# Optimization experiments

Hardware: AMD Instinct MI355X
Metric: run time of the kernel (lower is better)

The kernel has to match this reference:

```python
import jax, jax.numpy as jnp
import numpy as np

N_NODES = 100000
F_DIM = 128      # graph.num_node_features
TE_DIM = 32      # te_emb_dim
D = F_DIM + TE_DIM  # attention embed_dim = 160
B = 4096         # number of target nodes (batched python loop)
K = 64           # candidates per target
TAU = 1.0
THRESHOLD = 0.2
EPS = 1e-10


def setup_inputs() -> dict:
    key = jax.random.key(0)
    ks = jax.random.split(key, 16)
    inp = {
        "x": jax.random.normal(ks[0], (N_NODES, F_DIM), dtype=jnp.float32),
        "target_node_ids": jax.random.randint(ks[1], (B,), 0, N_NODES),
        "target_node_times": jax.random.randint(ks[2], (B,), 1, 10000),
        "neighbor_ids": jax.random.randint(ks[3], (B, K), 0, N_NODES),
        "edge_time": jax.random.randint(ks[4], (B, K), 0, 10000),
        "edge_weight": jax.random.uniform(ks[5], (B, K), dtype=jnp.float32),
        "gumbel_u": jax.random.uniform(ks[6], (B, K), dtype=jnp.float32),
        # TemporalEncoding params: te(t) = cos(t * w + b)
        "te_w": jax.random.normal(ks[7], (TE_DIM,), dtype=jnp.float32),
        "te_b": jax.random.normal(ks[8], (TE_DIM,), dtype=jnp.float32),
        # MultiheadAttention params (packed qkv like torch)
        "in_proj_w": jax.random.normal(ks[9], (3 * D, D), dtype=jnp.float32) / np.sqrt(D),
        "in_proj_b": jnp.zeros((3 * D,), dtype=jnp.float32),
        "out_w": jax.random.normal(ks[10], (D, D), dtype=jnp.float32) / np.sqrt(D),
        "out_b": jnp.zeros((D,), dtype=jnp.float32),
        # MLP: Linear(D+1 -> 1) + LeakyReLU
        "mlp_w": jax.random.normal(ks[11], (D + 1,), dtype=jnp.float32) / np.sqrt(D + 1),
        "mlp_b": jnp.zeros((1,), dtype=jnp.float32),
    }
    return inp


def reference(x, target_node_ids, target_node_times, neighbor_ids, edge_time,
              edge_weight, gumbel_u, te_w, te_b, in_proj_w, in_proj_b,
              out_w, out_b, mlp_w, mlp_b):
    # --- build target embedding: [B, D]
    t_x = x[target_node_ids]                                          # [B, F]
    t_te = jnp.cos(target_node_times[:, None].astype(jnp.float32) * te_w + te_b)  # [B, TE]
    q_in = jnp.concatenate([t_x, t_te], axis=-1)                      # [B, D]

    # --- candidate embeddings: [B, K, D]
    c_x = x[neighbor_ids]                                             # [B, K, F]
    c_te = jnp.cos(edge_time[..., None].astype(jnp.float32) * te_w + te_b)        # [B, K, TE]
    kv_in = jnp.concatenate([c_x, c_te], axis=-1)                     # [B, K, D]

    # --- single-head MultiheadAttention (eval mode, 1 query per target)
    Wq, Wk, Wv = in_proj_w[:D], in_proj_w[D:2 * D], in_proj_w[2 * D:]
    bq, bk, bv = in_proj_b[:D], in_proj_b[D:2 * D], in_proj_b[2 * D:]
    q = q_in @ Wq.T + bq                                              # [B, D]
    k = jnp.einsum('bkf,df->bkd', kv_in, Wk) + bk                     # [B, K, D]
    v = jnp.einsum('bkf,df->bkd', kv_in, Wv) + bv                     # [B, K, D]
    scores = jnp.einsum('bd,bkd->bk', q, k) / jnp.sqrt(jnp.float32(D))
    attn_w = jax.nn.softmax(scores, axis=-1)                          # [B, K]
    ctx = jnp.einsum('bk,bkd->bd', attn_w, v)                         # [B, D]
    attn_output = ctx @ out_w.T + out_b                               # [B, D]

    # --- gumbel-softmax mask over attention weights (soft, then threshold)
    g = -jnp.log(-jnp.log(gumbel_u + EPS) + EPS)                      # gumbel(0,1)
    y_soft = jax.nn.softmax((attn_w + g) / TAU, axis=-1)
    candidate_mask = y_soft > THRESHOLD                               # [B, K] bool

    # --- MLP edge-weight update: Linear(D+1 -> 1) + LeakyReLU
    mlp_in = jnp.concatenate(
        [jnp.broadcast_to(attn_output[:, None, :], (attn_output.shape[0], edge_weight.shape[1], attn_output.shape[1])),
         edge_weight[..., None]], axis=-1)                            # [B, K, D+1]
    new_edge_weight = jax.nn.leaky_relu(jnp.einsum('bkf,f->bk', mlp_in, mlp_w) + mlp_b[0])  # [B, K]

    return attn_output, new_edge_weight, candidate_mask
```

## Files before the change

kernel.cpp:

```cpp
#include <hip/hip_runtime.h>

#define F_DIM 128
#define TE_DIM 32
#define DD 160
#define NB 4096
#define KK 64
#define ROWS 4
#define LD 164
#define TE_STRIDE 36

#define WS_M   0
#define WS_V2  25600
#define WS_C   51200
#define WS_U   51360
#define WS_B2  51520
#define WS_S0  51680
#define WS_TE  51684
#define TAB_T  10000
#define TAB_N  (TAB_T * TE_DIM)
#define TAB_BLOCKS 250
#define SETUP_BASE (2 * DD + 3)

__device__ __forceinline__ float dot4acc(const float4 w, const float4 v, float a) {
    a = fmaf(w.x, v.x, a);
    a = fmaf(w.y, v.y, a);
    a = fmaf(w.z, v.z, a);
    a = fmaf(w.w, v.w, a);
    return a;
}

__device__ __forceinline__ float wave_max(float v) {
    #pragma unroll
    for (int off = 32; off > 0; off >>= 1) v = fmaxf(v, __shfl_xor(v, off, 64));
    return v;
}
__device__ __forceinline__ float wave_sum(float v) {
    #pragma unroll
    for (int off = 32; off > 0; off >>= 1) v += __shfl_xor(v, off, 64);
    return v;
}

__device__ __forceinline__ void gemv_rows(
    const float* __restrict__ W, const float* __restrict__ bias,
    const float (*vin)[LD], float (*vout)[LD], int tid)
{
    const int r  = tid & 3;
    const int dl = tid >> 2;
    const float4* v4 = (const float4*)vin[r];
    const float4* w0 = (const float4*)(W + (long)dl * DD);
    const float4* w1 = (const float4*)(W + (long)(dl + 64) * DD);
    float a0 = bias[dl];
    float a1 = bias[dl + 64];
    if (dl < 32) {
        const float4* w2 = (const float4*)(W + (long)(dl + 128) * DD);
        float a2 = bias[dl + 128];
        #pragma unroll 8
        for (int f = 0; f < 40; ++f) {
            const float4 v = v4[f];
            a0 = dot4acc(w0[f], v, a0);
            a1 = dot4acc(w1[f], v, a1);
            a2 = dot4acc(w2[f], v, a2);
        }
        vout[r][dl]       = a0;
        vout[r][dl + 64]  = a1;
        vout[r][dl + 128] = a2;
    } else {
        #pragma unroll 8
        for (int f = 0; f < 40; ++f) {
            const float4 v = v4[f];
            a0 = dot4acc(w0[f], v, a0);
            a1 = dot4acc(w1[f], v, a1);
        }
        vout[r][dl]      = a0;
        vout[r][dl + 64] = a1;
    }
}

__global__ __launch_bounds__(256)
void setup_kernel(const float* __restrict__ ipw, const float* __restrict__ ipb,
                  const float* __restrict__ ow,  const float* __restrict__ ob,
                  const float* __restrict__ te_w, const float* __restrict__ te_b,
                  float* __restrict__ ws)
{
    const int blk = blockIdx.x;
    const int t   = threadIdx.x;
    const float inv = 0.07905694150420949f;

    __shared__ float s_vec[DD];

    if (blk >= SETUP_BASE) {
        const int g0 = (blk - SETUP_BASE) * 256 + t;
        #pragma unroll
        for (int it = 0; it < 5; ++it) {
            const int g = g0 + it * (TAB_BLOCKS * 256);
            const int tt = g >> 5, d = g & 31;
            ws[WS_TE + g] = cosf(fmaf((float)tt, te_w[d], te_b[d]));
        }
        return;
    }

    if (blk < DD) {
        const float* wk = ipw + DD * DD;
        if (t < DD) s_vec[t] = wk[(long)t * DD + blk];
        __syncthreads();
        if (t < DD) {
            float a0 = 0.f, a1 = 0.f, a2 = 0.f, a3 = 0.f;
            #pragma unroll 4
            for (int d = 0; d < DD; d += 4) {
                a0 = fmaf(s_vec[d],     ipw[(long)d * DD + t],       a0);
                a1 = fmaf(s_vec[d + 1], ipw[(long)(d + 1) * DD + t], a1);
                a2 = fmaf(s_vec[d + 2], ipw[(long)(d + 2) * DD + t], a2);
                a3 = fmaf(s_vec[d + 3], ipw[(long)(d + 3) * DD + t], a3);
            }
            ws[WS_M + blk * DD + t] = (a0 + a1 + a2 + a3) * inv;
        }
    } else if (blk < 2 * DD) {
        const int i = blk - DD;
        const float* wv = ipw + 2 * DD * DD;
        if (t < DD) s_vec[t] = ow[(long)i * DD + t];
        __syncthreads();
        if (t < DD) {
            float a0 = 0.f, a1 = 0.f, a2 = 0.f, a3 = 0.f;
            #pragma unroll 4
            for (int d = 0; d < DD; d += 4) {
                a0 = fmaf(s_vec[d],     wv[(long)d * DD + t],       a0);
                a1 = fmaf(s_vec[d + 1], wv[(long)(d + 1) * DD + t], a1);
                a2 = fmaf(s_vec[d + 2], wv[(long)(d + 2) * DD + t], a2);
                a3 = fmaf(s_vec[d + 3], wv[(long)(d + 3) * DD + t], a3);
            }
            ws[WS_V2 + i * DD + t] = a0 + a1 + a2 + a3;
        }
    } else if (blk == 2 * DD) {
        const float* wk = ipw + DD * DD;
        if (t < DD) s_vec[t] = ipb[t];
        __syncthreads();
        if (t < DD) {
            float a0 = 0.f, a1 = 0.f, a2 = 0.f, a3 = 0.f;
            #pragma unroll 4
            for (int d = 0; d < DD; d += 4) {
                a0 = fmaf(s_vec[d],     wk[(long)d * DD + t],       a0);
                a1 = fmaf(s_vec[d + 1], wk[(long)(d + 1) * DD + t], a1);
                a2 = fmaf(s_vec[d + 2], wk[(long)(d + 2) * DD + t], a2);
                a3 = fmaf(s_vec[d + 3], wk[(long)(d + 3) * DD + t], a3);
            }
            ws[WS_C + t] = (a0 + a1 + a2 + a3) * inv;
        }
    } else if (blk == 2 * DD + 1) {
        if (t < DD) s_vec[t] = ipb[DD + t];
        __syncthreads();
        if (t < DD) {
            float a0 = 0.f, a1 = 0.f, a2 = 0.f, a3 = 0.f;
            #pragma unroll 4
            for (int d = 0; d < DD; d += 4) {
                a0 = fmaf(s_vec[d],     ipw[(long)d * DD + t],       a0);
                a1 = fmaf(s_vec[d + 1], ipw[(long)(d + 1) * DD + t], a1);
                a2 = fmaf(s_vec[d + 2], ipw[(long)(d + 2) * DD + t], a2);
                a3 = fmaf(s_vec[d + 3], ipw[(long)(d + 3) * DD + t], a3);
            }
            ws[WS_U + t] = (a0 + a1 + a2 + a3) * inv;
        }
    } else {
        if (t < DD) s_vec[t] = ipb[2 * DD + t];
        __syncthreads();
        if (t < DD) {
            const float* owr = ow + (long)t * DD;
            float a0 = 0.f, a1 = 0.f, a2 = 0.f, a3 = 0.f;
            #pragma unroll 4
            for (int d = 0; d < DD; d += 4) {
                a0 = fmaf(s_vec[d],     owr[d],     a0);
                a1 = fmaf(s_vec[d + 1], owr[d + 1], a1);
                a2 = fmaf(s_vec[d + 2], owr[d + 2], a2);
                a3 = fmaf(s_vec[d + 3], owr[d + 3], a3);
            }
            ws[WS_B2 + t] = ob[t] + (a0 + a1 + a2 + a3);
        }
        if (t >= 192) {
            const int lane = t - 192;
            float p = ipb[lane] * ipb[DD + lane];
            p = fmaf(ipb[lane + 64], ipb[DD + lane + 64], p);
            if (lane < 32) p = fmaf(ipb[lane + 128], ipb[DD + lane + 128], p);
            const float s = wave_sum(p);
            if (lane == 0) ws[WS_S0] = s * inv;
        }
    }
}

__global__ __launch_bounds__(256, 4)
void structure_learner_kernel(
    const float* __restrict__ x,
    const int*   __restrict__ target_node_ids,
    const int*   __restrict__ target_node_times,
    const int*   __restrict__ neighbor_ids,
    const int*   __restrict__ edge_time,
    const float* __restrict__ edge_weight,
    const float* __restrict__ gumbel_u,
    const float* __restrict__ te_w,
    const float* __restrict__ te_b,
    const float* __restrict__ mlp_w,
    const float* __restrict__ mlp_b,
    const float* __restrict__ ws,
    const float* __restrict__ tetab,
    float* __restrict__ out_ao,
    float* __restrict__ out_new,
    float* __restrict__ out_mask)
{
    __shared__ __attribute__((aligned(16))) float s_qin[ROWS][LD];
    __shared__ __attribute__((aligned(16))) float s_qt[ROWS][LD];
    __shared__ __attribute__((aligned(16))) float s_wkv[ROWS][LD];
    __shared__ __attribute__((aligned(16))) float s_ao[ROWS][LD];
    __shared__ float s_attnw[ROWS][KK];
    __shared__ int   s_nid[ROWS][KK];
    __shared__ __attribute__((aligned(4))) _Float16 s_te[ROWS][KK][TE_STRIDE];

    const int tid  = threadIdx.x;
    const int wr   = tid >> 6;
    const int lane = tid & 63;
    const int b    = blockIdx.x * ROWS + wr;

    const float* Mw = ws + WS_M;
    const float* V2 = ws + WS_V2;
    const float* Cv = ws + WS_C;
    const float* Uv = ws + WS_U;
    const float* B2 = ws + WS_B2;
    const float  s0 = ws[WS_S0];

    {
        s_nid[wr][lane] = neighbor_ids[(long)b * KK + lane];
        const int etv_i = edge_time[(long)b * KK + lane];
        const int tn = target_node_ids[b];
        const float2 tx = *(const float2*)(x + (long)tn * F_DIM + lane * 2);
        s_qin[wr][lane * 2]     = tx.x;
        s_qin[wr][lane * 2 + 1] = tx.y;
        if (lane < TE_DIM) {
            const int tt = target_node_times[b];
            s_qin[wr][F_DIM + lane] =
                (tetab && (unsigned)tt < (unsigned)TAB_T)
                    ? tetab[(long)tt * TE_DIM + lane]
                    : cosf(fmaf((float)tt, te_w[lane], te_b[lane]));
        }
        if (tetab && (unsigned)etv_i < (unsigned)TAB_T) {
            const float4* trow = (const float4*)(tetab + (long)etv_i * TE_DIM);
            #pragma unroll
            for (int jj = 0; jj < 8; ++jj) {
                const float4 tv = trow[jj];
                union { _Float16 h[2]; unsigned u; } p0, p1;
                p0.h[0] = (_Float16)tv.x; p0.h[1] = (_Float16)tv.y;
                p1.h[0] = (_Float16)tv.z; p1.h[1] = (_Float16)tv.w;
                *(unsigned*)&s_te[wr][lane][4 * jj]     = p0.u;
                *(unsigned*)&s_te[wr][lane][4 * jj + 2] = p1.u;
            }
        } else {
            const float etv = (float)etv_i;
            #pragma unroll
            for (int jj = 0; jj < 16; ++jj) {
                union { _Float16 h[2]; unsigned u; } pk;
                pk.h[0] = (_Float16)cosf(fmaf(etv, te_w[2 * jj],     te_b[2 * jj]));
                pk.h[1] = (_Float16)cosf(fmaf(etv, te_w[2 * jj + 1], te_b[2 * jj + 1]));
                *(unsigned*)&s_te[wr][lane][2 * jj] = pk.u;
            }
        }
    }
    __syncthreads();

    gemv_rows(Mw, Cv, s_qin, s_qt, tid);
    __syncthreads();

    float aw;
    {
        float p = s_qin[wr][lane] * Uv[lane];
        p = fmaf(s_qin[wr][lane + 64], Uv[lane + 64], p);
        if (lane < 32) p = fmaf(s_qin[wr][128 + lane], Uv[128 + lane], p);
        const float sbk = wave_sum(p) + s0;

        const int nidk = s_nid[wr][lane];
        const float4* xr  = (const float4*)(x + (long)nidk * F_DIM);
        const float4* qt4 = (const float4*)s_qt[wr];
        float acc0 = 0.f, acc1 = 0.f;
        #pragma unroll 16
        for (int f = 0; f < F_DIM / 8; ++f) {
            acc0 = dot4acc(xr[2 * f],     qt4[2 * f],     acc0);
            acc1 = dot4acc(xr[2 * f + 1], qt4[2 * f + 1], acc1);
        }
        float acc = acc0 + acc1;
        const float* qte = s_qt[wr] + F_DIM;
        #pragma unroll
        for (int jj = 0; jj < 16; ++jj) {
            union { _Float16 h[2]; unsigned u; } pk;
            pk.u = *(const unsigned*)&s_te[wr][lane][2 * jj];
            acc = fmaf(qte[2 * jj],     (float)pk.h[0], acc);
            acc = fmaf(qte[2 * jj + 1], (float)pk.h[1], acc);
        }
        const float sc = acc + sbk;
        const float m = wave_max(sc);
        const float e = expf(sc - m);
        const float l = wave_sum(e);
        aw = e / l;
        s_attnw[wr][lane] = aw;
    }

    {
        float ax = 0.f, ay = 0.f, at = 0.f;
        const float* xb = x + lane * 2;
        const int lte = lane & 31;
        #pragma unroll 16
        for (int k = 0; k < KK; ++k) {
            const float wgt = s_attnw[wr][k];
            const int   nid = s_nid[wr][k];
            const float2 xv = *(const float2*)(xb + (long)nid * F_DIM);
            ax = fmaf(wgt, xv.x, ax);
            ay = fmaf(wgt, xv.y, ay);
            at = fmaf(wgt, (float)s_te[wr][k][lte], at);
        }
        s_wkv[wr][lane * 2]     = ax;
        s_wkv[wr][lane * 2 + 1] = ay;
        if (lane < TE_DIM) s_wkv[wr][F_DIM + lane] = at;
    }
    __syncthreads();

    gemv_rows(V2, B2, s_wkv, s_ao, tid);
    __syncthreads();

    {
        float p = s_ao[wr][lane] * mlp_w[lane];
        p = fmaf(s_ao[wr][lane + 64], mlp_w[lane + 64], p);
        if (lane < 32) p = fmaf(s_ao[wr][lane + 128], mlp_w[lane + 128], p);
        const float base = wave_sum(p) + mlp_b[0];

        float* ao = out_ao + (long)b * DD;
        ao[lane]      = s_ao[wr][lane];
        ao[lane + 64] = s_ao[wr][lane + 64];
        if (lane < 32) ao[lane + 128] = s_ao[wr][lane + 128];

        const float u = gumbel_u[(long)b * KK + lane];
        const float g = -logf(-logf(u + 1e-10f) + 1e-10f);
        const float z = aw + g;
        const float m = wave_max(z);
        const float e = expf(z - m);
        const float l = wave_sum(e);
        out_mask[(long)b * KK + lane] = (e / l > 0.2f) ? 1.0f : 0.0f;

        const float ew  = edge_weight[(long)b * KK + lane];
        const float val = fmaf(ew, mlp_w[DD], base);
        out_new[(long)b * KK + lane] = (val >= 0.f) ? val : 0.01f * val;
    }
}

extern "C" void kernel_launch(void* const* d_in, const int* in_sizes, int n_in,
                              void* d_out, int out_size, void* d_ws, size_t ws_size,
                              hipStream_t stream) {
    const float* x   = (const float*)d_in[0];
    const int*   tni = (const int*)d_in[1];
    const int*   tnt = (const int*)d_in[2];
    const int*   nid = (const int*)d_in[3];
    const int*   et  = (const int*)d_in[4];
    const float* ew  = (const float*)d_in[5];
    const float* gu  = (const float*)d_in[6];
    const float* tew = (const float*)d_in[7];
    const float* teb = (const float*)d_in[8];
    const float* ipw = (const float*)d_in[9];
    const float* ipb = (const float*)d_in[10];
    const float* ow  = (const float*)d_in[11];
    const float* ob  = (const float*)d_in[12];
    const float* mw  = (const float*)d_in[13];
    const float* mb  = (const float*)d_in[14];

    float* wsf = (float*)d_ws;

    float* out      = (float*)d_out;
    float* out_ao   = out;
    float* out_new  = out + (long)NB * DD;
    float* out_mask = out + (long)NB * DD + (long)NB * KK;

    const bool use_tab = ws_size >= (size_t)(WS_TE + TAB_N) * sizeof(float);
    const int  setup_grid = SETUP_BASE + (use_tab ? TAB_BLOCKS : 0);

    setup_kernel<<<setup_grid, 256, 0, stream>>>(ipw, ipb, ow, ob, tew, teb, wsf);

    structure_learner_kernel<<<NB / ROWS, 256, 0, stream>>>(
        x, tni, tnt, nid, et, ew, gu, tew, teb, mw, mb, wsf,
        use_tab ? (wsf + WS_TE) : nullptr,
        out_ao, out_new, out_mask);
}
```

Before: 175.4 us.

## Software-pipeline neighbor row gathers across barriers and GEMV phases

The first chunk of each candidate's feature row is prefetched into registers before the barrier and first GEMV, and the rest is loaded in double-buffered chunks. The weighted-sum gather over neighbors is issued in batches of eight, with the first batch launched before the softmax reductions. The gumbel and edge-weight loads are hoisted ahead of the second GEMV. The aim is to hide global-memory gather latency behind compute and synchronisation, at the cost of higher register pressure that may reduce occupancy.

After: 175.8 us. No clear change (+0.2%).

```diff
diff --git a/kernel.cpp b/kernel.cpp
--- a/kernel.cpp
+++ b/kernel.cpp
@@ -224,8 +224,9 @@
     const float* B2 = ws + WS_B2;
     const float  s0 = ws[WS_S0];
 
+    const int nidk = neighbor_ids[(long)b * KK + lane];
     {
-        s_nid[wr][lane] = neighbor_ids[(long)b * KK + lane];
+        s_nid[wr][lane] = nidk;
         const int etv_i = edge_time[(long)b * KK + lane];
         const int tn = target_node_ids[b];
         const float2 tx = *(const float2*)(x + (long)tn * F_DIM + lane * 2);
@@ -260,6 +261,12 @@
             }
         }
     }
+
+    const float4* xr = (const float4*)(x + (long)nidk * F_DIM);
+    float4 cA[8];
+    #pragma unroll
+    for (int j = 0; j < 8; ++j) cA[j] = xr[j];
+
     __syncthreads();
 
     gemv_rows(Mw, Cv, s_qin, s_qt, tid);
@@ -267,21 +274,44 @@
 
     float aw;
     {
+        float4 cB[8];
+        #pragma unroll
+        for (int j = 0; j < 8; ++j) cB[j] = xr[8 + j];
+
         float p = s_qin[wr][lane] * Uv[lane];
         p = fmaf(s_qin[wr][lane + 64], Uv[lane + 64], p);
         if (lane < 32) p = fmaf(s_qin[wr][128 + lane], Uv[128 + lane], p);
         const float sbk = wave_sum(p) + s0;
 
-        const int nidk = s_nid[wr][lane];
-        const float4* xr  = (const float4*)(x + (long)nidk * F_DIM);
         const float4* qt4 = (const float4*)s_qt[wr];
         float acc0 = 0.f, acc1 = 0.f;
-        #pragma unroll 16
-        for (int f = 0; f < F_DIM / 8; ++f) {
-            acc0 = dot4acc(xr[2 * f],     qt4[2 * f],     acc0);
-            acc1 = dot4acc(xr[2 * f + 1], qt4[2 * f + 1], acc1);
+
+        #pragma unroll
+        for (int j = 0; j < 8; j += 2) {
+            acc0 = dot4acc(cA[j],     qt4[j],     acc0);
+            acc1 = dot4acc(cA[j + 1], qt4[j + 1], acc1);
+        }
+        #pragma unroll
+        for (int j = 0; j < 8; ++j) cA[j] = xr[16 + j];
+        #pragma unroll
+        for (int j = 0; j < 8; j += 2) {
+            acc0 = dot4acc(cB[j],     qt4[8 + j], acc0);
+            acc1 = dot4acc(cB[j + 1], qt4[9 + j], acc1);
+        }
+        #pragma unroll
+        for (int j = 0; j < 8; ++j) cB[j] = xr[24 + j];
+        #pragma unroll
+        for (int j = 0; j < 8; j += 2) {
+            acc0 = dot4acc(cA[j],     qt4[16 + j], acc0);
+            acc1 = dot4acc(cA[j + 1], qt4[17 + j], acc1);
+        }
+        #pragma unroll
+        for (int j = 0; j < 8; j += 2) {
+            acc0 = dot4acc(cB[j],     qt4[24 + j], acc0);
+            acc1 = dot4acc(cB[j + 1], qt4[25 + j], acc1);
         }
         float acc = acc0 + acc1;
+
         const float* qte = s_qt[wr] + F_DIM;
         #pragma unroll
         for (int jj = 0; jj < 16; ++jj) {
@@ -291,31 +321,47 @@
             acc = fmaf(qte[2 * jj + 1], (float)pk.h[1], acc);
         }
         const float sc = acc + sbk;
+
+        const float* xb = x + lane * 2;
+        float2 vc[8];
+        #pragma unroll
+        for (int j = 0; j < 8; ++j)
+            vc[j] = *(const float2*)(xb + (long)s_nid[wr][j] * F_DIM);
+
         const float m = wave_max(sc);
         const float e = expf(sc - m);
         const float l = wave_sum(e);
         aw = e / l;
         s_attnw[wr][lane] = aw;
-    }
-
-    {
+
         float ax = 0.f, ay = 0.f, at = 0.f;
-        const float* xb = x + lane * 2;
         const int lte = lane & 31;
-        #pragma unroll 16
-        for (int k = 0; k < KK; ++k) {
-            const float wgt = s_attnw[wr][k];
-            const int   nid = s_nid[wr][k];
-            const float2 xv = *(const float2*)(xb + (long)nid * F_DIM);
-            ax = fmaf(wgt, xv.x, ax);
-            ay = fmaf(wgt, xv.y, ay);
-            at = fmaf(wgt, (float)s_te[wr][k][lte], at);
+        #pragma unroll
+        for (int c = 0; c < 8; ++c) {
+            float2 vn[8];
+            if (c < 7) {
+                #pragma unroll
+                for (int j = 0; j < 8; ++j)
+                    vn[j] = *(const float2*)(xb + (long)s_nid[wr][(c + 1) * 8 + j] * F_DIM);
+            }
+            #pragma unroll
+            for (int j = 0; j < 8; ++j) {
+                const int k = c * 8 + j;
+                const float wgt = s_attnw[wr][k];
+                ax = fmaf(wgt, vc[j].x, ax);
+                ay = fmaf(wgt, vc[j].y, ay);
+                at = fmaf(wgt, (float)s_te[wr][k][lte], at);
+                if (c < 7) vc[j] = vn[j];
+            }
         }
         s_wkv[wr][lane * 2]     = ax;
         s_wkv[wr][lane * 2 + 1] = ay;
         if (lane < TE_DIM) s_wkv[wr][F_DIM + lane] = at;
     }
     __syncthreads();
+
+    const float u  = gumbel_u[(long)b * KK + lane];
+    const float ew = edge_weight[(long)b * KK + lane];
 
     gemv_rows(V2, B2, s_wkv, s_ao, tid);
     __syncthreads();
@@ -331,7 +377,6 @@
         ao[lane + 64] = s_ao[wr][lane + 64];
         if (lane < 32) ao[lane + 128] = s_ao[wr][lane + 128];
 
-        const float u = gumbel_u[(long)b * KK + lane];
         const float g = -logf(-logf(u + 1e-10f) + 1e-10f);
         const float z = aw + g;
         const float m = wave_max(z);
@@ -339,7 +384,6 @@
         const float l = wave_sum(e);
         out_mask[(long)b * KK + lane] = (e / l > 0.2f) ? 1.0f : 0.0f;
 
-        const float ew  = edge_weight[(long)b * KK + lane];
         const float val = fmaf(ew, mlp_w[DD], base);
         out_new[(long)b * KK + lane] = (val >= 0.f) ? val : 0.01f * val;
     }
```

## Split each target row across two waves with cross-wave softmax merge

Applied to the files above, without the earlier changes.

Each block now handles 2 target rows instead of 4, and each row is split across two waves. Each wave covers 32 candidates, with lane pairs splitting the feature dot products, and the two halves' softmax max and sum are merged through shared memory. The weighted-value sums are kept as two partial vectors that are added inside the output GEMV. This doubles the block count and raises the occupancy hint to 8, aiming to improve latency hiding for the gathered neighbor loads. The cost is extra __syncthreads and shared-memory reductions, plus each block re-reading the GEMV weights for fewer rows.

Result: slower. 234.5 us (+33.7%).

```diff
diff --git a/kernel.cpp b/kernel.cpp
--- a/kernel.cpp
+++ b/kernel.cpp
@@ -5,7 +5,7 @@
 #define DD 160
 #define NB 4096
 #define KK 64
-#define ROWS 4
+#define ROWS 2
 #define LD 164
 #define TE_STRIDE 36
 
@@ -44,35 +44,62 @@
     const float* __restrict__ W, const float* __restrict__ bias,
     const float (*vin)[LD], float (*vout)[LD], int tid)
 {
-    const int r  = tid & 3;
-    const int dl = tid >> 2;
+    const int r  = tid & 1;
+    const int dl = tid >> 1;
     const float4* v4 = (const float4*)vin[r];
     const float4* w0 = (const float4*)(W + (long)dl * DD);
-    const float4* w1 = (const float4*)(W + (long)(dl + 64) * DD);
     float a0 = bias[dl];
-    float a1 = bias[dl + 64];
     if (dl < 32) {
-        const float4* w2 = (const float4*)(W + (long)(dl + 128) * DD);
-        float a2 = bias[dl + 128];
+        const float4* w1 = (const float4*)(W + (long)(dl + 128) * DD);
+        float a1 = bias[dl + 128];
         #pragma unroll 8
         for (int f = 0; f < 40; ++f) {
             const float4 v = v4[f];
             a0 = dot4acc(w0[f], v, a0);
             a1 = dot4acc(w1[f], v, a1);
-            a2 = dot4acc(w2[f], v, a2);
         }
         vout[r][dl]       = a0;
-        vout[r][dl + 64]  = a1;
-        vout[r][dl + 128] = a2;
+        vout[r][dl + 128] = a1;
     } else {
         #pragma unroll 8
         for (int f = 0; f < 40; ++f) {
             const float4 v = v4[f];
             a0 = dot4acc(w0[f], v, a0);
+        }
+        vout[r][dl] = a0;
+    }
+}
+
+__device__ __forceinline__ void gemv_rows2(
+    const float* __restrict__ W, const float* __restrict__ bias,
+    const float (*vin)[2][LD], float (*vout)[LD], int tid)
+{
+    const int r  = tid & 1;
+    const int dl = tid >> 1;
+    const float4* va = (const float4*)vin[r][0];
+    const float4* vb = (const float4*)vin[r][1];
+    const float4* w0 = (const float4*)(W + (long)dl * DD);
+    float a0 = bias[dl];
+    if (dl < 32) {
+        const float4* w1 = (const float4*)(W + (long)(dl + 128) * DD);
+        float a1 = bias[dl + 128];
+        #pragma unroll 8
+        for (int f = 0; f < 40; ++f) {
+            const float4 A = va[f], B = vb[f];
+            float4 v; v.x = A.x + B.x; v.y = A.y + B.y; v.z = A.z + B.z; v.w = A.w + B.w;
+            a0 = dot4acc(w0[f], v, a0);
             a1 = dot4acc(w1[f], v, a1);
         }
-        vout[r][dl]      = a0;
-        vout[r][dl + 64] = a1;
+        vout[r][dl]       = a0;
+        vout[r][dl + 128] = a1;
+    } else {
+        #pragma unroll 8
+        for (int f = 0; f < 40; ++f) {
+            const float4 A = va[f], B = vb[f];
+            float4 v; v.x = A.x + B.x; v.y = A.y + B.y; v.z = A.z + B.z; v.w = A.w + B.w;
+            a0 = dot4acc(w0[f], v, a0);
+        }
+        vout[r][dl] = a0;
     }
 }
 
@@ -185,7 +212,7 @@
     }
 }
 
-__global__ __launch_bounds__(256, 4)
+__global__ __launch_bounds__(256, 8)
 void structure_learner_kernel(
     const float* __restrict__ x,
     const int*   __restrict__ target_node_ids,
@@ -206,15 +233,22 @@
 {
     __shared__ __attribute__((aligned(16))) float s_qin[ROWS][LD];
     __shared__ __attribute__((aligned(16))) float s_qt[ROWS][LD];
-    __shared__ __attribute__((aligned(16))) float s_wkv[ROWS][LD];
+    __shared__ __attribute__((aligned(16))) float s_wkvh[ROWS][2][LD];
     __shared__ __attribute__((aligned(16))) float s_ao[ROWS][LD];
     __shared__ float s_attnw[ROWS][KK];
     __shared__ int   s_nid[ROWS][KK];
     __shared__ __attribute__((aligned(4))) _Float16 s_te[ROWS][KK][TE_STRIDE];
+    __shared__ float2 s_red[ROWS][2];
+    __shared__ float2 s_red2[ROWS][2];
 
     const int tid  = threadIdx.x;
-    const int wr   = tid >> 6;
+    const int w    = tid >> 6;
     const int lane = tid & 63;
+    const int wr   = w >> 1;
+    const int h    = w & 1;
+    const int kk   = lane >> 1;
+    const int j    = lane & 1;
+    const int k    = h * 32 + kk;
     const int b    = blockIdx.x * ROWS + wr;
 
     const float* Mw = ws + WS_M;
@@ -225,38 +259,44 @@
     const float  s0 = ws[WS_S0];
 
     {
-        s_nid[wr][lane] = neighbor_ids[(long)b * KK + lane];
-        const int etv_i = edge_time[(long)b * KK + lane];
-        const int tn = target_node_ids[b];
-        const float2 tx = *(const float2*)(x + (long)tn * F_DIM + lane * 2);
-        s_qin[wr][lane * 2]     = tx.x;
-        s_qin[wr][lane * 2 + 1] = tx.y;
-        if (lane < TE_DIM) {
+        if (lane < 32) {
+            const int km = h * 32 + lane;
+            s_nid[wr][km] = neighbor_ids[(long)b * KK + km];
+        }
+        if (h == 0) {
+            const int tn = target_node_ids[b];
+            const float2 tx = *(const float2*)(x + (long)tn * F_DIM + lane * 2);
+            s_qin[wr][lane * 2]     = tx.x;
+            s_qin[wr][lane * 2 + 1] = tx.y;
+        } else if (lane < TE_DIM) {
             const int tt = target_node_times[b];
             s_qin[wr][F_DIM + lane] =
                 (tetab && (unsigned)tt < (unsigned)TAB_T)
                     ? tetab[(long)tt * TE_DIM + lane]
                     : cosf(fmaf((float)tt, te_w[lane], te_b[lane]));
         }
+        const int etv_i = edge_time[(long)b * KK + k];
         if (tetab && (unsigned)etv_i < (unsigned)TAB_T) {
-            const float4* trow = (const float4*)(tetab + (long)etv_i * TE_DIM);
+            const float4* trow = (const float4*)(tetab + (long)etv_i * TE_DIM) + 4 * j;
             #pragma unroll
-            for (int jj = 0; jj < 8; ++jj) {
-                const float4 tv = trow[jj];
-                union { _Float16 h[2]; unsigned u; } p0, p1;
-                p0.h[0] = (_Float16)tv.x; p0.h[1] = (_Float16)tv.y;
-                p1.h[0] = (_Float16)tv.z; p1.h[1] = (_Float16)tv.w;
-                *(unsigned*)&s_te[wr][lane][4 * jj]     = p0.u;
-                *(unsigned*)&s_te[wr][lane][4 * jj + 2] = p1.u;
+            for (int q = 0; q < 4; ++q) {
+                const float4 tv = trow[q];
+                const int jj = 4 * j + q;
+                union { _Float16 h2[2]; unsigned u; } p0, p1;
+                p0.h2[0] = (_Float16)tv.x; p0.h2[1] = (_Float16)tv.y;
+                p1.h2[0] = (_Float16)tv.z; p1.h2[1] = (_Float16)tv.w;
+                *(unsigned*)&s_te[wr][k][4 * jj]     = p0.u;
+                *(unsigned*)&s_te[wr][k][4 * jj + 2] = p1.u;
             }
         } else {
             const float etv = (float)etv_i;
             #pragma unroll
-            for (int jj = 0; jj < 16; ++jj) {
-                union { _Float16 h[2]; unsigned u; } pk;
-                pk.h[0] = (_Float16)cosf(fmaf(etv, te_w[2 * jj],     te_b[2 * jj]));
-                pk.h[1] = (_Float16)cosf(fmaf(etv, te_w[2 * jj + 1], te_b[2 * jj + 1]));
-                *(unsigned*)&s_te[wr][lane][2 * jj] = pk.u;
+            for (int q = 0; q < 8; ++q) {
+                const int d0 = 16 * j + 2 * q;
+                union { _Float16 h2[2]; unsigned u; } pk;
+                pk.h2[0] = (_Float16)cosf(fmaf(etv, te_w[d0],     te_b[d0]));
+                pk.h2[1] = (_Float16)cosf(fmaf(etv, te_w[d0 + 1], te_b[d0 + 1]));
+                *(unsigned*)&s_te[wr][k][d0] = pk.u;
             }
         }
     }
@@ -265,83 +305,107 @@
     gemv_rows(Mw, Cv, s_qin, s_qt, tid);
     __syncthreads();
 
-    float aw;
+    float e_loc, m_h;
     {
         float p = s_qin[wr][lane] * Uv[lane];
         p = fmaf(s_qin[wr][lane + 64], Uv[lane + 64], p);
         if (lane < 32) p = fmaf(s_qin[wr][128 + lane], Uv[128 + lane], p);
         const float sbk = wave_sum(p) + s0;
 
-        const int nidk = s_nid[wr][lane];
-        const float4* xr  = (const float4*)(x + (long)nidk * F_DIM);
-        const float4* qt4 = (const float4*)s_qt[wr];
+        const int nidk = s_nid[wr][k];
+        const float4* xr  = (const float4*)(x + (long)nidk * F_DIM) + 16 * j;
+        const float4* qt4 = (const float4*)s_qt[wr] + 16 * j;
         float acc0 = 0.f, acc1 = 0.f;
-        #pragma unroll 16
-        for (int f = 0; f < F_DIM / 8; ++f) {
-            acc0 = dot4acc(xr[2 * f],     qt4[2 * f],     acc0);
-            acc1 = dot4acc(xr[2 * f + 1], qt4[2 * f + 1], acc1);
+        #pragma unroll 8
+        for (int f = 0; f < 16; f += 2) {
+            acc0 = dot4acc(xr[f],     qt4[f],     acc0);
+            acc1 = dot4acc(xr[f + 1], qt4[f + 1], acc1);
         }
         float acc = acc0 + acc1;
-        const float* qte = s_qt[wr] + F_DIM;
+        const float* qte = s_qt[wr] + F_DIM + 16 * j;
         #pragma unroll
-        for (int jj = 0; jj < 16; ++jj) {
-            union { _Float16 h[2]; unsigned u; } pk;
-            pk.u = *(const unsigned*)&s_te[wr][lane][2 * jj];
-            acc = fmaf(qte[2 * jj],     (float)pk.h[0], acc);
-            acc = fmaf(qte[2 * jj + 1], (float)pk.h[1], acc);
-        }
+        for (int ii = 0; ii < 8; ++ii) {
+            union { _Float16 h2[2]; unsigned u; } pk;
+            pk.u = *(const unsigned*)&s_te[wr][k][16 * j + 2 * ii];
+            acc = fmaf(qte[2 * ii],     (float)pk.h2[0], acc);
+            acc = fmaf(qte[2 * ii + 1], (float)pk.h2[1], acc);
+        }
+        acc += __shfl_xor(acc, 1, 64);
         const float sc = acc + sbk;
-        const float m = wave_max(sc);
-        const float e = expf(sc - m);
-        const float l = wave_sum(e);
-        aw = e / l;
-        s_attnw[wr][lane] = aw;
-    }
-
+        m_h = wave_max(sc);
+        e_loc = expf(sc - m_h);
+        const float l_h = wave_sum(e_loc) * 0.5f;
+        if (lane == 0) s_red[wr][h] = make_float2(m_h, l_h);
+    }
+    __syncthreads();
+
+    float aw;
     {
+        const float2 R0 = s_red[wr][0], R1 = s_red[wr][1];
+        const float m = fmaxf(R0.x, R1.x);
+        const float l = R0.y * expf(R0.x - m) + R1.y * expf(R1.x - m);
+        aw = e_loc * expf(m_h - m) / l;
+        if (j == 0) s_attnw[wr][k] = aw;
+
         float ax = 0.f, ay = 0.f, at = 0.f;
         const float* xb = x + lane * 2;
         const int lte = lane & 31;
-        #pragma unroll 16
-        for (int k = 0; k < KK; ++k) {
-            const float wgt = s_attnw[wr][k];
-            const int   nid = s_nid[wr][k];
+        #pragma unroll 8
+        for (int q = 0; q < 32; ++q) {
+            const int kq = 32 * h + q;
+            const float wgt = s_attnw[wr][kq];
+            const int   nid = s_nid[wr][kq];
             const float2 xv = *(const float2*)(xb + (long)nid * F_DIM);
             ax = fmaf(wgt, xv.x, ax);
             ay = fmaf(wgt, xv.y, ay);
-            at = fmaf(wgt, (float)s_te[wr][k][lte], at);
-        }
-        s_wkv[wr][lane * 2]     = ax;
-        s_wkv[wr][lane * 2 + 1] = ay;
-        if (lane < TE_DIM) s_wkv[wr][F_DIM + lane] = at;
-    }
-    __syncthreads();
-
-    gemv_rows(V2, B2, s_wkv, s_ao, tid);
-    __syncthreads();
-
+            at = fmaf(wgt, (float)s_te[wr][kq][lte], at);
+        }
+        s_wkvh[wr][h][lane * 2]     = ax;
+        s_wkvh[wr][h][lane * 2 + 1] = ay;
+        if (lane < TE_DIM) s_wkvh[wr][h][F_DIM + lane] = at;
+    }
+    __syncthreads();
+
+    const float u  = gumbel_u[(long)b * KK + k];
+    const float ew = edge_weight[(long)b * KK + k];
+
+    gemv_rows2(V2, B2, s_wkvh, s_ao, tid);
+    __syncthreads();
+
+    float base, y_e, y_mh;
     {
         float p = s_ao[wr][lane] * mlp_w[lane];
         p = fmaf(s_ao[wr][lane + 64], mlp_w[lane + 64], p);
         if (lane < 32) p = fmaf(s_ao[wr][lane + 128], mlp_w[lane + 128], p);
-        const float base = wave_sum(p) + mlp_b[0];
+        base = wave_sum(p) + mlp_b[0];
 
         float* ao = out_ao + (long)b * DD;
-        ao[lane]      = s_ao[wr][lane];
-        ao[lane + 64] = s_ao[wr][lane + 64];
-        if (lane < 32) ao[lane + 128] = s_ao[wr][lane + 128];
-
-        const float u = gumbel_u[(long)b * KK + lane];
+        if (h == 0) {
+            ao[lane] = s_ao[wr][lane];
+            if (lane < 32) ao[128 + lane] = s_ao[wr][128 + lane];
+        } else {
+            ao[64 + lane] = s_ao[wr][64 + lane];
+        }
+
         const float g = -logf(-logf(u + 1e-10f) + 1e-10f);
         const float z = aw + g;
-        const float m = wave_max(z);
-        const float e = expf(z - m);
-        const float l = wave_sum(e);
-        out_mask[(long)b * KK + lane] = (e / l > 0.2f) ? 1.0f : 0.0f;
-
-        const float ew  = edge_weight[(long)b * KK + lane];
-        const float val = fmaf(ew, mlp_w[DD], base);
-        out_new[(long)b * KK + lane] = (val >= 0.f) ? val : 0.01f * val;
+        y_mh = wave_max(z);
+        y_e  = expf(z - y_mh);
+        const float l_h = wave_sum(y_e) * 0.5f;
+        if (lane == 0) s_red2[wr][h] = make_float2(y_mh, l_h);
+    }
+    __syncthreads();
+
+    {
+        const float2 R0 = s_red2[wr][0], R1 = s_red2[wr][1];
+        const float m = fmaxf(R0.x, R1.x);
+        const float l = R0.y * expf(R0.x - m) + R1.y * expf(R1.x - m);
+        const float y = y_e * expf(y_mh - m) / l;
+        if (j == 0) {
+            out_mask[(long)b * KK + k] = (y > 0.2f) ? 1.0f : 0.0f;
+            const float val = fmaf(ew, mlp_w[DD], base);
+            out_new[(long)b * KK + k] = (val >= 0.f) ? val : 0.01f * val;
+        }
     }
 }
 
```

## Fuse score and weighted-sum passes with online softmax over fp16 staged neighbor tiles

Applied to the files above, without the earlier changes.

The kernel now processes candidates in tiles of 16, with 4 lanes per candidate. Each neighbor's x row and temporal encoding is loaded from global memory once, used for the score dot product, and staged as fp16 in shared memory for the attention-weighted accumulation. An online-softmax rescale replaces the separate full softmax, and the second global gather of x rows is gone. In exchange it adds block-wide syncs per tile, rounds x to fp16 in the context sum, and reconstructs the attention weights afterwards for the gumbel mask.

After: 162.4 us, median of 2. 7.4% less time.

```diff
diff --git a/kernel.cpp b/kernel.cpp
--- a/kernel.cpp
+++ b/kernel.cpp
@@ -7,7 +7,8 @@
 #define KK 64
 #define ROWS 4
 #define LD 164
-#define TE_STRIDE 36
+#define XH_STRIDE 168
+#define KT 16
 
 #define WS_M   0
 #define WS_V2  25600
@@ -204,13 +205,15 @@
     float* __restrict__ out_new,
     float* __restrict__ out_mask)
 {
+    __shared__ __attribute__((aligned(16))) _Float16 s_xh[ROWS][KT][XH_STRIDE];
     __shared__ __attribute__((aligned(16))) float s_qin[ROWS][LD];
     __shared__ __attribute__((aligned(16))) float s_qt[ROWS][LD];
     __shared__ __attribute__((aligned(16))) float s_wkv[ROWS][LD];
     __shared__ __attribute__((aligned(16))) float s_ao[ROWS][LD];
-    __shared__ float s_attnw[ROWS][KK];
+    __shared__ float s_aw[ROWS][KK];
+    __shared__ float s_mt[ROWS][4];
     __shared__ int   s_nid[ROWS][KK];
-    __shared__ __attribute__((aligned(4))) _Float16 s_te[ROWS][KK][TE_STRIDE];
+    __shared__ int   s_et[ROWS][KK];
 
     const int tid  = threadIdx.x;
     const int wr   = tid >> 6;
@@ -225,8 +228,9 @@
     const float  s0 = ws[WS_S0];
 
     {
-        s_nid[wr][lane] = neighbor_ids[(long)b * KK + lane];
-        const int etv_i = edge_time[(long)b * KK + lane];
+        const long eb = (long)b * KK + lane;
+        s_nid[wr][lane] = neighbor_ids[eb];
+        s_et[wr][lane]  = edge_time[eb];
         const int tn = target_node_ids[b];
         const float2 tx = *(const float2*)(x + (long)tn * F_DIM + lane * 2);
         s_qin[wr][lane * 2]     = tx.x;
@@ -238,108 +242,137 @@
                     ? tetab[(long)tt * TE_DIM + lane]
                     : cosf(fmaf((float)tt, te_w[lane], te_b[lane]));
         }
-        if (tetab && (unsigned)etv_i < (unsigned)TAB_T) {
-            const float4* trow = (const float4*)(tetab + (long)etv_i * TE_DIM);
-            #pragma unroll
-            for (int jj = 0; jj < 8; ++jj) {
-                const float4 tv = trow[jj];
-                union { _Float16 h[2]; unsigned u; } p0, p1;
-                p0.h[0] = (_Float16)tv.x; p0.h[1] = (_Float16)tv.y;
-                p1.h[0] = (_Float16)tv.z; p1.h[1] = (_Float16)tv.w;
-                *(unsigned*)&s_te[wr][lane][4 * jj]     = p0.u;
-                *(unsigned*)&s_te[wr][lane][4 * jj + 2] = p1.u;
-            }
-        } else {
-            const float etv = (float)etv_i;
-            #pragma unroll
-            for (int jj = 0; jj < 16; ++jj) {
-                union { _Float16 h[2]; unsigned u; } pk;
-                pk.h[0] = (_Float16)cosf(fmaf(etv, te_w[2 * jj],     te_b[2 * jj]));
-                pk.h[1] = (_Float16)cosf(fmaf(etv, te_w[2 * jj + 1], te_b[2 * jj + 1]));
-                *(unsigned*)&s_te[wr][lane][2 * jj] = pk.u;
-            }
-        }
     }
     __syncthreads();
 
     gemv_rows(Mw, Cv, s_qin, s_qt, tid);
     __syncthreads();
 
-    float aw;
-    {
-        float p = s_qin[wr][lane] * Uv[lane];
-        p = fmaf(s_qin[wr][lane + 64], Uv[lane + 64], p);
-        if (lane < 32) p = fmaf(s_qin[wr][128 + lane], Uv[128 + lane], p);
-        const float sbk = wave_sum(p) + s0;
-
-        const int nidk = s_nid[wr][lane];
-        const float4* xr  = (const float4*)(x + (long)nidk * F_DIM);
-        const float4* qt4 = (const float4*)s_qt[wr];
-        float acc0 = 0.f, acc1 = 0.f;
-        #pragma unroll 16
-        for (int f = 0; f < F_DIM / 8; ++f) {
-            acc0 = dot4acc(xr[2 * f],     qt4[2 * f],     acc0);
-            acc1 = dot4acc(xr[2 * f + 1], qt4[2 * f + 1], acc1);
-        }
-        float acc = acc0 + acc1;
-        const float* qte = s_qt[wr] + F_DIM;
+    float p = s_qin[wr][lane] * Uv[lane];
+    p = fmaf(s_qin[wr][lane + 64], Uv[lane + 64], p);
+    if (lane < 32) p = fmaf(s_qin[wr][128 + lane], Uv[128 + lane], p);
+    const float sbk = wave_sum(p) + s0;
+
+    const int q = lane >> 2;
+    const int j = lane & 3;
+    float m_run = -3.0e38f, l_run = 0.f;
+    float ax = 0.f, ay = 0.f, at = 0.f;
+
+    for (int t = 0; t < 4; ++t) {
+        const int k   = KT * t + q;
+        const int nid = s_nid[wr][k];
+        const int et  = s_et[wr][k];
+
+        const float4* xr  = (const float4*)(x + (long)nid * F_DIM + 32 * j);
+        const float4* qt4 = (const float4*)(s_qt[wr] + 32 * j);
+        _Float16* st = &s_xh[wr][q][32 * j];
+        float a0 = 0.f, a1 = 0.f;
         #pragma unroll
-        for (int jj = 0; jj < 16; ++jj) {
-            union { _Float16 h[2]; unsigned u; } pk;
-            pk.u = *(const unsigned*)&s_te[wr][lane][2 * jj];
-            acc = fmaf(qte[2 * jj],     (float)pk.h[0], acc);
-            acc = fmaf(qte[2 * jj + 1], (float)pk.h[1], acc);
-        }
+        for (int f = 0; f < 8; f += 2) {
+            const float4 A = xr[f], B = xr[f + 1];
+            a0 = dot4acc(A, qt4[f],     a0);
+            a1 = dot4acc(B, qt4[f + 1], a1);
+            union { _Float16 hh[4]; unsigned long long u; } pa, pb;
+            pa.hh[0] = (_Float16)A.x; pa.hh[1] = (_Float16)A.y;
+            pa.hh[2] = (_Float16)A.z; pa.hh[3] = (_Float16)A.w;
+            pb.hh[0] = (_Float16)B.x; pb.hh[1] = (_Float16)B.y;
+            pb.hh[2] = (_Float16)B.z; pb.hh[3] = (_Float16)B.w;
+            *(unsigned long long*)&st[4 * f]     = pa.u;
+            *(unsigned long long*)&st[4 * f + 4] = pb.u;
+        }
+        float acc = a0 + a1;
+
+        {
+            const float* qte = s_qt[wr] + F_DIM + 8 * j;
+            _Float16* stt = &s_xh[wr][q][F_DIM + 8 * j];
+            if (tetab && (unsigned)et < (unsigned)TAB_T) {
+                const float4* tr = (const float4*)(tetab + (long)et * TE_DIM + 8 * j);
+                const float4 T0 = tr[0], T1 = tr[1];
+                acc = fmaf(T0.x, qte[0], acc);
+                acc = fmaf(T0.y, qte[1], acc);
+                acc = fmaf(T0.z, qte[2], acc);
+                acc = fmaf(T0.w, qte[3], acc);
+                acc = fmaf(T1.x, qte[4], acc);
+                acc = fmaf(T1.y, qte[5], acc);
+                acc = fmaf(T1.z, qte[6], acc);
+                acc = fmaf(T1.w, qte[7], acc);
+                union { _Float16 hh[4]; unsigned long long u; } p0, p1;
+                p0.hh[0] = (_Float16)T0.x; p0.hh[1] = (_Float16)T0.y;
+                p0.hh[2] = (_Float16)T0.z; p0.hh[3] = (_Float16)T0.w;
+                p1.hh[0] = (_Float16)T1.x; p1.hh[1] = (_Float16)T1.y;
+                p1.hh[2] = (_Float16)T1.z; p1.hh[3] = (_Float16)T1.w;
+                *(unsigned long long*)&stt[0] = p0.u;
+                *(unsigned long long*)&stt[4] = p1.u;
+            } else {
+                const float etv = (float)et;
+                #pragma unroll
+                for (int ii = 0; ii < 8; ++ii) {
+                    const float cte = cosf(fmaf(etv, te_w[8 * j + ii], te_b[8 * j + ii]));
+                    acc = fmaf(cte, qte[ii], acc);
+                    stt[ii] = (_Float16)cte;
+                }
+            }
+        }
+
+        acc += __shfl_xor(acc, 1, 64);
+        acc += __shfl_xor(acc, 2, 64);
         const float sc = acc + sbk;
-        const float m = wave_max(sc);
-        const float e = expf(sc - m);
-        const float l = wave_sum(e);
-        aw = e / l;
-        s_attnw[wr][lane] = aw;
-    }
-
-    {
-        float ax = 0.f, ay = 0.f, at = 0.f;
-        const float* xb = x + lane * 2;
-        const int lte = lane & 31;
-        #pragma unroll 16
-        for (int k = 0; k < KK; ++k) {
-            const float wgt = s_attnw[wr][k];
-            const int   nid = s_nid[wr][k];
-            const float2 xv = *(const float2*)(xb + (long)nid * F_DIM);
-            ax = fmaf(wgt, xv.x, ax);
-            ay = fmaf(wgt, xv.y, ay);
-            at = fmaf(wgt, (float)s_te[wr][k][lte], at);
-        }
-        s_wkv[wr][lane * 2]     = ax;
-        s_wkv[wr][lane * 2 + 1] = ay;
-        if (lane < TE_DIM) s_wkv[wr][F_DIM + lane] = at;
-    }
+
+        const float mt   = wave_max(sc);
+        const float mnew = fmaxf(m_run, mt);
+        const float cfac = expf(m_run - mnew);
+        const float e    = expf(sc - mnew);
+        l_run = l_run * cfac + wave_sum(e) * 0.25f;
+        m_run = mnew;
+        if (j == 0)    s_aw[wr][k]  = e;
+        if (lane == 0) s_mt[wr][t]  = mnew;
+        __syncthreads();
+
+        ax *= cfac; ay *= cfac; at *= cfac;
+        #pragma unroll
+        for (int qq = 0; qq < KT; ++qq) {
+            const float wgt = s_aw[wr][KT * t + qq];
+            union { unsigned u; _Float16 h2[2]; } cc;
+            cc.u = *(const unsigned*)&s_xh[wr][qq][2 * lane];
+            ax = fmaf(wgt, (float)cc.h2[0], ax);
+            ay = fmaf(wgt, (float)cc.h2[1], ay);
+            if (lane < TE_DIM) at = fmaf(wgt, (float)s_xh[wr][qq][F_DIM + lane], at);
+        }
+        __syncthreads();
+    }
+
+    const float rl = 1.f / l_run;
+    s_wkv[wr][lane * 2]     = ax * rl;
+    s_wkv[wr][lane * 2 + 1] = ay * rl;
+    if (lane < TE_DIM) s_wkv[wr][F_DIM + lane] = at * rl;
+
+    const float u  = gumbel_u[(long)b * KK + lane];
+    const float ew = edge_weight[(long)b * KK + lane];
     __syncthreads();
 
     gemv_rows(V2, B2, s_wkv, s_ao, tid);
     __syncthreads();
 
     {
-        float p = s_ao[wr][lane] * mlp_w[lane];
-        p = fmaf(s_ao[wr][lane + 64], mlp_w[lane + 64], p);
-        if (lane < 32) p = fmaf(s_ao[wr][lane + 128], mlp_w[lane + 128], p);
-        const float base = wave_sum(p) + mlp_b[0];
+        const float awk = s_aw[wr][lane] * expf(s_mt[wr][lane >> 4] - m_run) * rl;
+
+        float pm = s_ao[wr][lane] * mlp_w[lane];
+        pm = fmaf(s_ao[wr][lane + 64], mlp_w[lane + 64], pm);
+        if (lane < 32) pm = fmaf(s_ao[wr][lane + 128], mlp_w[lane + 128], pm);
+        const float base = wave_sum(pm) + mlp_b[0];
 
         float* ao = out_ao + (long)b * DD;
         ao[lane]      = s_ao[wr][lane];
         ao[lane + 64] = s_ao[wr][lane + 64];
         if (lane < 32) ao[lane + 128] = s_ao[wr][lane + 128];
 
-        const float u = gumbel_u[(long)b * KK + lane];
         const float g = -logf(-logf(u + 1e-10f) + 1e-10f);
-        const float z = aw + g;
+        const float z = awk + g;
         const float m = wave_max(z);
         const float e = expf(z - m);
         const float l = wave_sum(e);
         out_mask[(long)b * KK + lane] = (e / l > 0.2f) ? 1.0f : 0.0f;
 
-        const float ew  = edge_weight[(long)b * KK + lane];
         const float val = fmaf(ew, mlp_w[DD], base);
         out_new[(long)b * KK + lane] = (val >= 0.f) ? val : 0.01f * val;
     }
```
